# Kernel tuning notes

Hardware: AMD Instinct MI355X
Metric: run time of the kernel (lower is better)

Reference implementation:

```python
import jax, jax.numpy as jnp
import numpy as np

N_EMBED = 384
NUM_HEADS = 6
HEAD_SIZE = 64
B, T = 128, 256


def setup_inputs() -> dict:
    key = jax.random.key(0)
    ks = jax.random.split(key, 6)
    x = jax.random.normal(ks[0], (B, T, N_EMBED), dtype=jnp.float32)
    s = 0.02
    Wq = jax.random.normal(ks[1], (NUM_HEADS, N_EMBED, HEAD_SIZE), dtype=jnp.float32) * s
    Wk = jax.random.normal(ks[2], (NUM_HEADS, N_EMBED, HEAD_SIZE), dtype=jnp.float32) * s
    Wv = jax.random.normal(ks[3], (NUM_HEADS, N_EMBED, HEAD_SIZE), dtype=jnp.float32) * s
    Wp = jax.random.normal(ks[4], (NUM_HEADS * HEAD_SIZE, N_EMBED), dtype=jnp.float32) * s
    bp = jnp.zeros((N_EMBED,), dtype=jnp.float32)
    return {"x": x, "Wq": Wq, "Wk": Wk, "Wv": Wv, "Wp": Wp, "bp": bp}


def reference(x, Wq, Wk, Wv, Wp, bp):
    # x: [B,T,C]; Wq/Wk/Wv: [H,C,hs]; Wp: [H*hs, C]
    Bx, Tx, C = x.shape
    q = jnp.einsum('btc,hcd->bhtd', x, Wq)
    k = jnp.einsum('btc,hcd->bhtd', x, Wk)
    v = jnp.einsum('btc,hcd->bhtd', x, Wv)
    scale = HEAD_SIZE ** (-0.5)
    scores = jnp.einsum('bhtd,bhsd->bhts', q, k) * scale  # [B,H,T,T]
    causal = jnp.tril(jnp.ones((Tx, Tx), dtype=bool))
    scores = jnp.where(causal, scores, -jnp.inf)
    attn = jax.nn.softmax(scores, axis=-1)
    # dropout is identity in eval mode
    out = jnp.einsum('bhts,bhsd->bhtd', attn, v)  # [B,H,T,hs]
    out = out.transpose(0, 2, 1, 3).reshape(Bx, Tx, NUM_HEADS * HEAD_SIZE)
    return out @ Wp + bp
```

## Files before the change

kernel.cpp:

```cpp
#include <hip/hip_runtime.h>
#include <hip/hip_bf16.h>

#define C_DIM 384
#define H_NUM 6
#define HS    64
#define B_DIM 128
#define T_DIM 256
#define NROWS (B_DIM * T_DIM)

typedef unsigned short u16;
typedef unsigned int u32;
typedef short bf16x8 __attribute__((ext_vector_type(8)));
typedef float floatx4 __attribute__((ext_vector_type(4)));

__device__ __forceinline__ float b2f(u16 u) {
  u32 i = ((u32)u) << 16;
  float f;
  __builtin_memcpy(&f, &i, 4);
  return f;
}
__device__ __forceinline__ u16 f2b(float f) {
  __hip_bfloat16 h = __float2bfloat16(f);
  u16 u;
  __builtin_memcpy(&u, &h, 2);
  return u;
}
__device__ __forceinline__ void gload_lds16(const void* g, void* lds) {
  __builtin_amdgcn_global_load_lds(
      (const __attribute__((address_space(1))) u32*)g,
      (__attribute__((address_space(3))) u32*)lds, 16, 0, 0);
}

__global__ void cvt_x_kernel(const float* __restrict__ x, u16* __restrict__ xb,
                             int n4) {
  int i = blockIdx.x * blockDim.x + threadIdx.x;
  if (i >= n4) return;
  float4 f = ((const float4*)x)[i];
  ushort4 o;
  o.x = f2b(f.x); o.y = f2b(f.y); o.z = f2b(f.z); o.w = f2b(f.w);
  ((ushort4*)xb)[i] = o;
}

__global__ void cvt_w_kernel(const float* __restrict__ Wq,
                             const float* __restrict__ Wk,
                             const float* __restrict__ Wv,
                             const float* __restrict__ Wp,
                             u16* __restrict__ Wt, u16* __restrict__ Wpt) {
  const int QKV = 3 * H_NUM * HS * C_DIM;
  int idx = blockIdx.x * blockDim.x + threadIdx.x;
  if (idx < QKV) {
    int slab = idx / (HS * C_DIM);
    int rem = idx % (HS * C_DIM);
    int d = rem / C_DIM, c = rem % C_DIM;
    int tz = slab / H_NUM, h = slab % H_NUM;
    const float* W = (tz == 0) ? Wq : (tz == 1) ? Wk : Wv;
    Wt[idx] = f2b(W[(h * C_DIM + c) * HS + d]);
  } else {
    int j = idx - QKV;
    if (j < C_DIM * C_DIM) {
      int n = j / C_DIM, c = j % C_DIM;
      Wpt[j] = f2b(Wp[c * C_DIM + n]);
    }
  }
}

struct GemmAcc {
  floatx4 acc[4][4];
};

__device__ __forceinline__ void gemm_tile_128x128(
    const u16* __restrict__ a_rows, const u16* __restrict__ bt_rows,
    u16* As, u16* Bs, GemmAcc& g) {
  const int tid = threadIdx.x;
  const int lane = tid & 63;
  const int w = tid >> 6;
  const int lr = lane >> 3;
  const int lkc = (lane & 7) * 8;
  const int qd = lane >> 4;
  const int ln = lane & 15;
  const int mw = (w >> 1) * 64;
  const int nw = (w & 1) * 64;

#pragma unroll
  for (int i = 0; i < 4; ++i)
#pragma unroll
    for (int j = 0; j < 4; ++j) g.acc[i][j] = floatx4{0.f, 0.f, 0.f, 0.f};

  for (int kb = 0; kb < C_DIM / 64; ++kb) {
    const int k0 = kb * 64;
    __syncthreads();
#pragma unroll
    for (int s = 0; s < 4; ++s) {
      const int rbase = (s * 4 + w) * 8;
      gload_lds16(a_rows + (size_t)(rbase + lr) * C_DIM + k0 + lkc,
                  As + rbase * 64);
      gload_lds16(bt_rows + (size_t)(rbase + lr) * C_DIM + k0 + lkc,
                  Bs + rbase * 64);
    }
    __syncthreads();

#pragma unroll
    for (int kk = 0; kk < 2; ++kk) {
      bf16x8 af[4], bf[4];
#pragma unroll
      for (int mt = 0; mt < 4; ++mt)
        af[mt] = *(const bf16x8*)&As[(mw + mt * 16 + ln) * 64 + kk * 32 + qd * 8];
#pragma unroll
      for (int nt = 0; nt < 4; ++nt)
        bf[nt] = *(const bf16x8*)&Bs[(nw + nt * 16 + ln) * 64 + kk * 32 + qd * 8];
#pragma unroll
      for (int mt = 0; mt < 4; ++mt)
#pragma unroll
        for (int nt = 0; nt < 4; ++nt)
          g.acc[mt][nt] = __builtin_amdgcn_mfma_f32_16x16x32_bf16(
              af[mt], bf[nt], g.acc[mt][nt], 0, 0, 0);
    }
  }
}

__global__ __launch_bounds__(256) void qkv_gemm(
    const u16* __restrict__ xb, const u16* __restrict__ Wt,
    u16* __restrict__ q, u16* __restrict__ k, u16* __restrict__ vT) {
  __shared__ u16 smem[128 * 136];
  u16* As = smem;
  u16* Bs = smem + 8192;
  const int row0 = blockIdx.x * 128;
  const int sb = blockIdx.y;
  const int tz = sb / 3;
  const int h0 = (sb % 3) * 2;
  const u16* wbase = Wt + (size_t)(tz * H_NUM + h0) * (HS * C_DIM);

  GemmAcc g;
  gemm_tile_128x128(xb + (size_t)row0 * C_DIM, wbase, As, Bs, g);

  const int lane = threadIdx.x & 63;
  const int w = threadIdx.x >> 6;
  const int qd = lane >> 4, ln = lane & 15;
  const int mw = (w >> 1) * 64, nw = (w & 1) * 64;

  if (tz < 2) {
    u16* outbase = (tz == 0) ? q : k;
#pragma unroll
    for (int mt = 0; mt < 4; ++mt) {
#pragma unroll
      for (int nt = 0; nt < 4; ++nt) {
        const int cl = nw + nt * 16 + ln;
        const int head = h0 + (cl >> 6), d = cl & 63;
#pragma unroll
        for (int r = 0; r < 4; ++r) {
          const int grow = row0 + mw + mt * 16 + qd * 4 + r;
          const int b = grow >> 8, t = grow & 255;
          outbase[(((size_t)b * H_NUM + head) * T_DIM + t) * HS + d] =
              f2b(g.acc[mt][nt][r]);
        }
      }
    }
  } else {
    __syncthreads();
#pragma unroll
    for (int mt = 0; mt < 4; ++mt)
#pragma unroll
      for (int nt = 0; nt < 4; ++nt)
#pragma unroll
        for (int r = 0; r < 4; ++r)
          smem[(nw + nt * 16 + ln) * 136 + mw + mt * 16 + qd * 4 + r] =
              f2b(g.acc[mt][nt][r]);
    __syncthreads();
    const int b = row0 >> 8;
    const int t0 = row0 & 255;
#pragma unroll
    for (int it = 0; it < 8; ++it) {
      const int idx = it * 256 + threadIdx.x;
      const int d_l = idx >> 4, tc = idx & 15;
      uint4 val = *(const uint4*)&smem[d_l * 136 + tc * 8];
      const int head = h0 + (d_l >> 6), d = d_l & 63;
      *(uint4*)&vT[(((size_t)b * H_NUM + head) * HS + d) * T_DIM + t0 + tc * 8] =
          val;
    }
  }
}

template <bool DIAG>
__device__ __forceinline__ void attn_chunk(int c, int mt, int lane, int ln,
                                           int qd, const bf16x8* qf,
                                           const u16* Kls, u16* Pw,
                                           const u16* vTg, floatx4* oacc,
                                           float* lsum) {
  floatx4 sacc[4];
#pragma unroll
  for (int st = 0; st < 4; ++st) {
    sacc[st] = floatx4{0.f, 0.f, 0.f, 0.f};
#pragma unroll
    for (int kc = 0; kc < 2; ++kc) {
      bf16x8 kf = *(const bf16x8*)&Kls[((c * 4 + st) * 2 + kc) * 512 + lane * 8];
      sacc[st] =
          __builtin_amdgcn_mfma_f32_16x16x32_bf16(qf[kc], kf, sacc[st], 0, 0, 0);
    }
  }
#pragma unroll
  for (int st = 0; st < 4; ++st) {
#pragma unroll
    for (int r = 0; r < 4; ++r) {
      const float sv = sacc[st][r] * 0.125f;
      float p = __expf(sv);
      if (DIAG) {
        const bool ok = (c * 64 + st * 16 + ln) <= (mt * 16 + qd * 4 + r);
        p = ok ? p : 0.f;
      }
      lsum[r] += p;
      Pw[(qd * 4 + r) * 72 + st * 16 + ln] = f2b(p);
    }
  }
#pragma unroll
  for (int kc2 = 0; kc2 < 2; ++kc2) {
    bf16x8 pf = *(const bf16x8*)&Pw[ln * 72 + kc2 * 32 + qd * 8];
#pragma unroll
    for (int dt = 0; dt < 4; ++dt) {
      bf16x8 vf = *(const bf16x8*)(vTg + (dt * 16 + ln) * 256 + c * 64 +
                                   kc2 * 32 + qd * 8);
      oacc[dt] =
          __builtin_amdgcn_mfma_f32_16x16x32_bf16(pf, vf, oacc[dt], 0, 0, 0);
    }
  }
}

__global__ __launch_bounds__(256) void attn_mfma(
    const u16* __restrict__ q, const u16* __restrict__ k,
    const u16* __restrict__ vT, u16* __restrict__ y) {
  __shared__ u16 Kls[32 * 512];
  __shared__ u16 Pls[4 * 1152];
  const int bh = blockIdx.x;
  const int b = bh / H_NUM, h = bh % H_NUM;
  const int tid = threadIdx.x, lane = tid & 63, w = tid >> 6;
  const int ln = lane & 15, qd = lane >> 4;
  const u16* qg = q + (size_t)bh * (T_DIM * HS);
  const u16* kg = k + (size_t)bh * (T_DIM * HS);
  const u16* vTg = vT + (size_t)bh * (HS * T_DIM);
  u16* Pw = Pls + w * 1152;

#pragma unroll
  for (int ff = 0; ff < 8; ++ff) {
    const int fid = w * 8 + ff;
    const int S16 = fid >> 1, kc = fid & 1;
    gload_lds16(kg + (S16 * 16 + ln) * 64 + kc * 32 + qd * 8, &Kls[fid * 512]);
  }
  __syncthreads();

#pragma unroll
  for (int i = 0; i < 4; ++i) {
    const int mt = i * 4 + w;
    bf16x8 qf[2];
#pragma unroll
    for (int kc = 0; kc < 2; ++kc)
      qf[kc] = *(const bf16x8*)(qg + (mt * 16 + ln) * 64 + kc * 32 + qd * 8);

    floatx4 oacc[4];
    float lsum[4];
#pragma unroll
    for (int dt = 0; dt < 4; ++dt) oacc[dt] = floatx4{0.f, 0.f, 0.f, 0.f};
#pragma unroll
    for (int r = 0; r < 4; ++r) lsum[r] = 0.f;

    const int cmax = mt >> 2;
    for (int c = 0; c < cmax; ++c)
      attn_chunk<false>(c, mt, lane, ln, qd, qf, Kls, Pw, vTg, oacc, lsum);
    attn_chunk<true>(cmax, mt, lane, ln, qd, qf, Kls, Pw, vTg, oacc, lsum);

#pragma unroll
    for (int off = 1; off < 16; off <<= 1)
#pragma unroll
      for (int r = 0; r < 4; ++r) lsum[r] += __shfl_xor(lsum[r], off);

#pragma unroll
    for (int r = 0; r < 4; ++r) {
      const float inv = 1.f / lsum[r];
      const int t = mt * 16 + qd * 4 + r;
      u16* yo = y + ((size_t)b * T_DIM + t) * C_DIM + h * HS;
#pragma unroll
      for (int dt = 0; dt < 4; ++dt) yo[dt * 16 + ln] = f2b(oacc[dt][r] * inv);
    }
  }
}

__global__ __launch_bounds__(256) void proj_gemm(
    const u16* __restrict__ yb, const u16* __restrict__ Wpt,
    const float* __restrict__ bp, float* __restrict__ out) {
  __shared__ u16 As[128 * 64];
  __shared__ u16 Bs[128 * 64];
  const int row0 = blockIdx.x * 128;
  const int n0 = blockIdx.y * 128;

  GemmAcc g;
  gemm_tile_128x128(yb + (size_t)row0 * C_DIM, Wpt + (size_t)n0 * C_DIM, As, Bs, g);

  const int lane = threadIdx.x & 63;
  const int w = threadIdx.x >> 6;
  const int qd = lane >> 4, ln = lane & 15;
  const int mw = (w >> 1) * 64, nw = (w & 1) * 64;
#pragma unroll
  for (int nt = 0; nt < 4; ++nt) {
    const int col = n0 + nw + nt * 16 + ln;
    const float bias = bp[col];
#pragma unroll
    for (int mt = 0; mt < 4; ++mt) {
#pragma unroll
      for (int r = 0; r < 4; ++r) {
        const int grow = row0 + mw + mt * 16 + qd * 4 + r;
        out[(size_t)grow * C_DIM + col] = g.acc[mt][nt][r] + bias;
      }
    }
  }
}

extern "C" void kernel_launch(void* const* d_in, const int* in_sizes, int n_in,
                              void* d_out, int out_size, void* d_ws, size_t ws_size,
                              hipStream_t stream) {
  const float* x  = (const float*)d_in[0];
  const float* Wq = (const float*)d_in[1];
  const float* Wk = (const float*)d_in[2];
  const float* Wv = (const float*)d_in[3];
  const float* Wp = (const float*)d_in[4];
  const float* bp = (const float*)d_in[5];
  float* out = (float*)d_out;

  const size_t n_x = (size_t)NROWS * C_DIM;
  const size_t qkv_elems = (size_t)B_DIM * H_NUM * T_DIM * HS;

  u16* xb  = (u16*)d_ws;
  u16* Wt  = xb + n_x;
  u16* Wpt = Wt + 3 * H_NUM * HS * C_DIM;
  u16* q   = Wpt + C_DIM * C_DIM;
  u16* k   = q + qkv_elems;
  u16* vT  = k + qkv_elems;
  u16* y   = xb;

  cvt_x_kernel<<<(int)(n_x / 4 + 255) / 256, 256, 0, stream>>>(x, xb, (int)(n_x / 4));
  cvt_w_kernel<<<2304, 256, 0, stream>>>(Wq, Wk, Wv, Wp, Wt, Wpt);
  qkv_gemm<<<dim3(NROWS / 128, 9), 256, 0, stream>>>(xb, Wt, q, k, vT);
  attn_mfma<<<B_DIM * H_NUM, 256, 0, stream>>>(q, k, vT, y);
  proj_gemm<<<dim3(NROWS / 128, 3), 256, 0, stream>>>(y, Wpt, bp, out);
}
```

Before: 225.5 us.

## Fuse x conversion, QKV projection and causal attention into one per-head kernel

Replaces the separate x-conversion, QKV GEMM and attention kernels with one kernel per (batch, head). Each kernel converts fp32 x to bf16 while staging it into LDS, computes that head's Q, K and V with MFMA, writes them to workspace, then runs causal attention with 8 waves. Query tiles are paired (w and 15-w) so each wave gets a similar amount of causal work. This removes two launches and the bf16 x round trip through memory. In exchange, each batch's x is reread and reconverted by all six head blocks, and Q/K/V still go through global memory within the block.

```diff
diff --git a/kernel.cpp b/kernel.cpp
--- a/kernel.cpp
+++ b/kernel.cpp
@@ -13,12 +13,6 @@
 typedef short bf16x8 __attribute__((ext_vector_type(8)));
 typedef float floatx4 __attribute__((ext_vector_type(4)));
 
-__device__ __forceinline__ float b2f(u16 u) {
-  u32 i = ((u32)u) << 16;
-  float f;
-  __builtin_memcpy(&f, &i, 4);
-  return f;
-}
 __device__ __forceinline__ u16 f2b(float f) {
   __hip_bfloat16 h = __float2bfloat16(f);
   u16 u;
@@ -31,35 +25,216 @@
       (__attribute__((address_space(3))) u32*)lds, 16, 0, 0);
 }
 
-__global__ void cvt_x_kernel(const float* __restrict__ x, u16* __restrict__ xb,
-                             int n4) {
-  int i = blockIdx.x * blockDim.x + threadIdx.x;
-  if (i >= n4) return;
-  float4 f = ((const float4*)x)[i];
-  ushort4 o;
-  o.x = f2b(f.x); o.y = f2b(f.y); o.z = f2b(f.z); o.w = f2b(f.w);
-  ((ushort4*)xb)[i] = o;
-}
-
 __global__ void cvt_w_kernel(const float* __restrict__ Wq,
                              const float* __restrict__ Wk,
                              const float* __restrict__ Wv,
                              const float* __restrict__ Wp,
-                             u16* __restrict__ Wt, u16* __restrict__ Wpt) {
-  const int QKV = 3 * H_NUM * HS * C_DIM;
+                             u16* __restrict__ Wh, u16* __restrict__ Wpt) {
+  const int WHN = H_NUM * 192 * C_DIM;
   int idx = blockIdx.x * blockDim.x + threadIdx.x;
-  if (idx < QKV) {
-    int slab = idx / (HS * C_DIM);
-    int rem = idx % (HS * C_DIM);
-    int d = rem / C_DIM, c = rem % C_DIM;
-    int tz = slab / H_NUM, h = slab % H_NUM;
+  if (idx < WHN) {
+    int h = idx / (192 * C_DIM);
+    int rem = idx % (192 * C_DIM);
+    int r = rem / C_DIM, c = rem % C_DIM;
+    int tz = r >> 6, d = r & 63;
     const float* W = (tz == 0) ? Wq : (tz == 1) ? Wk : Wv;
-    Wt[idx] = f2b(W[(h * C_DIM + c) * HS + d]);
+    Wh[idx] = f2b(W[((size_t)h * C_DIM + c) * HS + d]);
   } else {
-    int j = idx - QKV;
+    int j = idx - WHN;
     if (j < C_DIM * C_DIM) {
       int n = j / C_DIM, c = j % C_DIM;
       Wpt[j] = f2b(Wp[c * C_DIM + n]);
+    }
+  }
+}
+
+template <bool DIAG>
+__device__ __forceinline__ void attn_chunk(int c, int mt, int lane, int ln,
+                                           int qd, const bf16x8* qf,
+                                           const u16* Kls, u16* Pw,
+                                           const u16* vTg, floatx4* oacc,
+                                           float* lsum) {
+  floatx4 sacc[4];
+#pragma unroll
+  for (int st = 0; st < 4; ++st) {
+    sacc[st] = floatx4{0.f, 0.f, 0.f, 0.f};
+#pragma unroll
+    for (int kc = 0; kc < 2; ++kc) {
+      bf16x8 kf = *(const bf16x8*)&Kls[((c * 4 + st) * 2 + kc) * 512 + lane * 8];
+      sacc[st] =
+          __builtin_amdgcn_mfma_f32_16x16x32_bf16(qf[kc], kf, sacc[st], 0, 0, 0);
+    }
+  }
+#pragma unroll
+  for (int st = 0; st < 4; ++st) {
+#pragma unroll
+    for (int r = 0; r < 4; ++r) {
+      const float sv = sacc[st][r] * 0.125f;
+      float p = __expf(sv);
+      if (DIAG) {
+        const bool ok = (c * 64 + st * 16 + ln) <= (mt * 16 + qd * 4 + r);
+        p = ok ? p : 0.f;
+      }
+      lsum[r] += p;
+      Pw[(qd * 4 + r) * 72 + st * 16 + ln] = f2b(p);
+    }
+  }
+#pragma unroll
+  for (int kc2 = 0; kc2 < 2; ++kc2) {
+    bf16x8 pf = *(const bf16x8*)&Pw[ln * 72 + kc2 * 32 + qd * 8];
+#pragma unroll
+    for (int dt = 0; dt < 4; ++dt) {
+      bf16x8 vf = *(const bf16x8*)(vTg + (dt * 16 + ln) * 256 + c * 64 +
+                                   kc2 * 32 + qd * 8);
+      oacc[dt] =
+          __builtin_amdgcn_mfma_f32_16x16x32_bf16(pf, vf, oacc[dt], 0, 0, 0);
+    }
+  }
+}
+
+__global__ __launch_bounds__(512, 4) void qkv_attn(
+    const float* __restrict__ x, const u16* __restrict__ Wh,
+    u16* __restrict__ qsA, u16* __restrict__ ksA, u16* __restrict__ vtA,
+    u16* __restrict__ y) {
+  __shared__ u16 smem[25600];
+  const int bh = blockIdx.x;
+  const int b = bh / H_NUM, h = bh % H_NUM;
+  const int tid = threadIdx.x, lane = tid & 63, w = tid >> 6;
+  const int qd = lane >> 4, ln = lane & 15;
+  const int wm = w & 1, wn = w >> 1;
+  const int lr = lane >> 3, lkc = (lane & 7) * 8;
+
+  const float* xb = x + (size_t)b * T_DIM * C_DIM;
+  const u16* Bh = Wh + (size_t)h * 192 * C_DIM;
+  u16* qs = qsA + (size_t)bh * (T_DIM * HS);
+  u16* ks = ksA + (size_t)bh * (T_DIM * HS);
+  u16* vt = vtA + (size_t)bh * (T_DIM * HS);
+
+  u16* As = smem;
+  u16* Bs = smem + 8192;
+  u16* Ts = smem;
+
+  for (int mh = 0; mh < 2; ++mh) {
+    const int t0 = mh * 128;
+    floatx4 acc[4][3];
+#pragma unroll
+    for (int mt = 0; mt < 4; ++mt)
+#pragma unroll
+      for (int nt = 0; nt < 3; ++nt) acc[mt][nt] = floatx4{0.f, 0.f, 0.f, 0.f};
+
+    for (int kb = 0; kb < 6; ++kb) {
+      const int k0 = kb * 64;
+      __syncthreads();
+#pragma unroll
+      for (int s = 0; s < 2; ++s) {
+        const int c = s * 512 + tid;
+        const int row = c >> 3, col = (c & 7) * 8;
+        const float* src = xb + (size_t)(t0 + row) * C_DIM + k0 + col;
+        const float4 f0 = *(const float4*)src;
+        const float4 f1 = *(const float4*)(src + 4);
+        bf16x8 pk;
+        pk[0] = (short)f2b(f0.x); pk[1] = (short)f2b(f0.y);
+        pk[2] = (short)f2b(f0.z); pk[3] = (short)f2b(f0.w);
+        pk[4] = (short)f2b(f1.x); pk[5] = (short)f2b(f1.y);
+        pk[6] = (short)f2b(f1.z); pk[7] = (short)f2b(f1.w);
+        *(bf16x8*)&As[row * 64 + col] = pk;
+      }
+#pragma unroll
+      for (int ss = 0; ss < 3; ++ss) {
+        const int rbase = (w * 3 + ss) * 8;
+        gload_lds16(Bh + (size_t)(rbase + lr) * C_DIM + k0 + lkc,
+                    Bs + rbase * 64);
+      }
+      __syncthreads();
+#pragma unroll
+      for (int kk = 0; kk < 2; ++kk) {
+        bf16x8 af[4], bfr[3];
+#pragma unroll
+        for (int mt = 0; mt < 4; ++mt)
+          af[mt] =
+              *(const bf16x8*)&As[(wm * 64 + mt * 16 + ln) * 64 + kk * 32 + qd * 8];
+#pragma unroll
+        for (int nt = 0; nt < 3; ++nt)
+          bfr[nt] =
+              *(const bf16x8*)&Bs[(wn * 48 + nt * 16 + ln) * 64 + kk * 32 + qd * 8];
+#pragma unroll
+        for (int mt = 0; mt < 4; ++mt)
+#pragma unroll
+          for (int nt = 0; nt < 3; ++nt)
+            acc[mt][nt] = __builtin_amdgcn_mfma_f32_16x16x32_bf16(
+                af[mt], bfr[nt], acc[mt][nt], 0, 0, 0);
+      }
+    }
+    __syncthreads();
+#pragma unroll
+    for (int nt = 0; nt < 3; ++nt) {
+      const int tz = (wn * 48 + nt * 16) >> 6;
+      const int d = (wn * 48 + nt * 16 + ln) & 63;
+#pragma unroll
+      for (int mt = 0; mt < 4; ++mt) {
+#pragma unroll
+        for (int r = 0; r < 4; ++r) {
+          const int tl = wm * 64 + mt * 16 + qd * 4 + r;
+          const u16 val = f2b(acc[mt][nt][r]);
+          if (tz == 0) qs[(size_t)(t0 + tl) * HS + d] = val;
+          else if (tz == 1) ks[(size_t)(t0 + tl) * HS + d] = val;
+          else Ts[d * 136 + tl] = val;
+        }
+      }
+    }
+    __syncthreads();
+#pragma unroll
+    for (int s = 0; s < 2; ++s) {
+      const int c = s * 512 + tid;
+      const int d = c >> 4, part = c & 15;
+      *(uint4*)&vt[(size_t)d * T_DIM + t0 + part * 8] =
+          *(const uint4*)&Ts[d * 136 + part * 8];
+    }
+  }
+  __syncthreads();
+
+  u16* Kls = smem;
+  u16* Pw = smem + 16384 + w * 1152;
+
+#pragma unroll
+  for (int ff = 0; ff < 4; ++ff) {
+    const int fid = w * 4 + ff, S16 = fid >> 1, kc = fid & 1;
+    gload_lds16(ks + (S16 * 16 + ln) * HS + kc * 32 + qd * 8, &Kls[fid * 512]);
+  }
+  __syncthreads();
+
+#pragma unroll
+  for (int i = 0; i < 2; ++i) {
+    const int mt = (i == 0) ? w : 15 - w;
+    bf16x8 qf[2];
+#pragma unroll
+    for (int kc = 0; kc < 2; ++kc)
+      qf[kc] = *(const bf16x8*)(qs + (mt * 16 + ln) * HS + kc * 32 + qd * 8);
+
+    floatx4 oacc[4];
+    float lsum[4];
+#pragma unroll
+    for (int dt = 0; dt < 4; ++dt) oacc[dt] = floatx4{0.f, 0.f, 0.f, 0.f};
+#pragma unroll
+    for (int r = 0; r < 4; ++r) lsum[r] = 0.f;
+
+    const int cmax = mt >> 2;
+    for (int c = 0; c < cmax; ++c)
+      attn_chunk<false>(c, mt, lane, ln, qd, qf, Kls, Pw, vt, oacc, lsum);
+    attn_chunk<true>(cmax, mt, lane, ln, qd, qf, Kls, Pw, vt, oacc, lsum);
+
+#pragma unroll
+    for (int off = 1; off < 16; off <<= 1)
+#pragma unroll
+      for (int r = 0; r < 4; ++r) lsum[r] += __shfl_xor(lsum[r], off);
+
+#pragma unroll
+    for (int r = 0; r < 4; ++r) {
+      const float inv = 1.f / lsum[r];
+      const int t = mt * 16 + qd * 4 + r;
+      u16* yo = y + ((size_t)b * T_DIM + t) * C_DIM + h * HS;
+#pragma unroll
+      for (int dt = 0; dt < 4; ++dt) yo[dt * 16 + ln] = f2b(oacc[dt][r] * inv);
     }
   }
 }
@@ -118,170 +293,6 @@
   }
 }
 
-__global__ __launch_bounds__(256) void qkv_gemm(
-    const u16* __restrict__ xb, const u16* __restrict__ Wt,
-    u16* __restrict__ q, u16* __restrict__ k, u16* __restrict__ vT) {
-  __shared__ u16 smem[128 * 136];
-  u16* As = smem;
-  u16* Bs = smem + 8192;
-  const int row0 = blockIdx.x * 128;
-  const int sb = blockIdx.y;
-  const int tz = sb / 3;
-  const int h0 = (sb % 3) * 2;
-  const u16* wbase = Wt + (size_t)(tz * H_NUM + h0) * (HS * C_DIM);
-
-  GemmAcc g;
-  gemm_tile_128x128(xb + (size_t)row0 * C_DIM, wbase, As, Bs, g);
-
-  const int lane = threadIdx.x & 63;
-  const int w = threadIdx.x >> 6;
-  const int qd = lane >> 4, ln = lane & 15;
-  const int mw = (w >> 1) * 64, nw = (w & 1) * 64;
-
-  if (tz < 2) {
-    u16* outbase = (tz == 0) ? q : k;
-#pragma unroll
-    for (int mt = 0; mt < 4; ++mt) {
-#pragma unroll
-      for (int nt = 0; nt < 4; ++nt) {
-        const int cl = nw + nt * 16 + ln;
-        const int head = h0 + (cl >> 6), d = cl & 63;
-#pragma unroll
-        for (int r = 0; r < 4; ++r) {
-          const int grow = row0 + mw + mt * 16 + qd * 4 + r;
-          const int b = grow >> 8, t = grow & 255;
-          outbase[(((size_t)b * H_NUM + head) * T_DIM + t) * HS + d] =
-              f2b(g.acc[mt][nt][r]);
-        }
-      }
-    }
-  } else {
-    __syncthreads();
-#pragma unroll
-    for (int mt = 0; mt < 4; ++mt)
-#pragma unroll
-      for (int nt = 0; nt < 4; ++nt)
-#pragma unroll
-        for (int r = 0; r < 4; ++r)
-          smem[(nw + nt * 16 + ln) * 136 + mw + mt * 16 + qd * 4 + r] =
-              f2b(g.acc[mt][nt][r]);
-    __syncthreads();
-    const int b = row0 >> 8;
-    const int t0 = row0 & 255;
-#pragma unroll
-    for (int it = 0; it < 8; ++it) {
-      const int idx = it * 256 + threadIdx.x;
-      const int d_l = idx >> 4, tc = idx & 15;
-      uint4 val = *(const uint4*)&smem[d_l * 136 + tc * 8];
-      const int head = h0 + (d_l >> 6), d = d_l & 63;
-      *(uint4*)&vT[(((size_t)b * H_NUM + head) * HS + d) * T_DIM + t0 + tc * 8] =
-          val;
-    }
-  }
-}
-
-template <bool DIAG>
-__device__ __forceinline__ void attn_chunk(int c, int mt, int lane, int ln,
-                                           int qd, const bf16x8* qf,
-                                           const u16* Kls, u16* Pw,
-                                           const u16* vTg, floatx4* oacc,
-                                           float* lsum) {
-  floatx4 sacc[4];
-#pragma unroll
-  for (int st = 0; st < 4; ++st) {
-    sacc[st] = floatx4{0.f, 0.f, 0.f, 0.f};
-#pragma unroll
-    for (int kc = 0; kc < 2; ++kc) {
-      bf16x8 kf = *(const bf16x8*)&Kls[((c * 4 + st) * 2 + kc) * 512 + lane * 8];
-      sacc[st] =
-          __builtin_amdgcn_mfma_f32_16x16x32_bf16(qf[kc], kf, sacc[st], 0, 0, 0);
-    }
-  }
-#pragma unroll
-  for (int st = 0; st < 4; ++st) {
-#pragma unroll
-    for (int r = 0; r < 4; ++r) {
-      const float sv = sacc[st][r] * 0.125f;
-      float p = __expf(sv);
-      if (DIAG) {
-        const bool ok = (c * 64 + st * 16 + ln) <= (mt * 16 + qd * 4 + r);
-        p = ok ? p : 0.f;
-      }
-      lsum[r] += p;
-      Pw[(qd * 4 + r) * 72 + st * 16 + ln] = f2b(p);
-    }
-  }
-#pragma unroll
-  for (int kc2 = 0; kc2 < 2; ++kc2) {
-    bf16x8 pf = *(const bf16x8*)&Pw[ln * 72 + kc2 * 32 + qd * 8];
-#pragma unroll
-    for (int dt = 0; dt < 4; ++dt) {
-      bf16x8 vf = *(const bf16x8*)(vTg + (dt * 16 + ln) * 256 + c * 64 +
-                                   kc2 * 32 + qd * 8);
-      oacc[dt] =
-          __builtin_amdgcn_mfma_f32_16x16x32_bf16(pf, vf, oacc[dt], 0, 0, 0);
-    }
-  }
-}
-
-__global__ __launch_bounds__(256) void attn_mfma(
-    const u16* __restrict__ q, const u16* __restrict__ k,
-    const u16* __restrict__ vT, u16* __restrict__ y) {
-  __shared__ u16 Kls[32 * 512];
-  __shared__ u16 Pls[4 * 1152];
-  const int bh = blockIdx.x;
-  const int b = bh / H_NUM, h = bh % H_NUM;
-  const int tid = threadIdx.x, lane = tid & 63, w = tid >> 6;
-  const int ln = lane & 15, qd = lane >> 4;
-  const u16* qg = q + (size_t)bh * (T_DIM * HS);
-  const u16* kg = k + (size_t)bh * (T_DIM * HS);
-  const u16* vTg = vT + (size_t)bh * (HS * T_DIM);
-  u16* Pw = Pls + w * 1152;
-
-#pragma unroll
-  for (int ff = 0; ff < 8; ++ff) {
-    const int fid = w * 8 + ff;
-    const int S16 = fid >> 1, kc = fid & 1;
-    gload_lds16(kg + (S16 * 16 + ln) * 64 + kc * 32 + qd * 8, &Kls[fid * 512]);
-  }
-  __syncthreads();
-
-#pragma unroll
-  for (int i = 0; i < 4; ++i) {
-    const int mt = i * 4 + w;
-    bf16x8 qf[2];
-#pragma unroll
-    for (int kc = 0; kc < 2; ++kc)
-      qf[kc] = *(const bf16x8*)(qg + (mt * 16 + ln) * 64 + kc * 32 + qd * 8);
-
-    floatx4 oacc[4];
-    float lsum[4];
-#pragma unroll
-    for (int dt = 0; dt < 4; ++dt) oacc[dt] = floatx4{0.f, 0.f, 0.f, 0.f};
-#pragma unroll
-    for (int r = 0; r < 4; ++r) lsum[r] = 0.f;
-
-    const int cmax = mt >> 2;
-    for (int c = 0; c < cmax; ++c)
-      attn_chunk<false>(c, mt, lane, ln, qd, qf, Kls, Pw, vTg, oacc, lsum);
-    attn_chunk<true>(cmax, mt, lane, ln, qd, qf, Kls, Pw, vTg, oacc, lsum);
-
-#pragma unroll
-    for (int off = 1; off < 16; off <<= 1)
-#pragma unroll
-      for (int r = 0; r < 4; ++r) lsum[r] += __shfl_xor(lsum[r], off);
-
-#pragma unroll
-    for (int r = 0; r < 4; ++r) {
-      const float inv = 1.f / lsum[r];
-      const int t = mt * 16 + qd * 4 + r;
-      u16* yo = y + ((size_t)b * T_DIM + t) * C_DIM + h * HS;
-#pragma unroll
-      for (int dt = 0; dt < 4; ++dt) yo[dt * 16 + ln] = f2b(oacc[dt][r] * inv);
-    }
-  }
-}
-
 __global__ __launch_bounds__(256) void proj_gemm(
     const u16* __restrict__ yb, const u16* __restrict__ Wpt,
     const float* __restrict__ bp, float* __restrict__ out) {
@@ -323,20 +334,16 @@
   const float* bp = (const float*)d_in[5];
   float* out = (float*)d_out;
 
-  const size_t n_x = (size_t)NROWS * C_DIM;
   const size_t qkv_elems = (size_t)B_DIM * H_NUM * T_DIM * HS;
 
-  u16* xb  = (u16*)d_ws;
-  u16* Wt  = xb + n_x;
-  u16* Wpt = Wt + 3 * H_NUM * HS * C_DIM;
-  u16* q   = Wpt + C_DIM * C_DIM;
-  u16* k   = q + qkv_elems;
-  u16* vT  = k + qkv_elems;
-  u16* y   = xb;
-
-  cvt_x_kernel<<<(int)(n_x / 4 + 255) / 256, 256, 0, stream>>>(x, xb, (int)(n_x / 4));
-  cvt_w_kernel<<<2304, 256, 0, stream>>>(Wq, Wk, Wv, Wp, Wt, Wpt);
-  qkv_gemm<<<dim3(NROWS / 128, 9), 256, 0, stream>>>(xb, Wt, q, k, vT);
-  attn_mfma<<<B_DIM * H_NUM, 256, 0, stream>>>(q, k, vT, y);
+  u16* Wh  = (u16*)d_ws;
+  u16* Wpt = Wh + (size_t)H_NUM * 192 * C_DIM;
+  u16* qsA = Wpt + C_DIM * C_DIM;
+  u16* ksA = qsA + qkv_elems;
+  u16* vtA = ksA + qkv_elems;
+  u16* y   = vtA + qkv_elems;
+
+  cvt_w_kernel<<<2304, 256, 0, stream>>>(Wq, Wk, Wv, Wp, Wh, Wpt);
+  qkv_attn<<<B_DIM * H_NUM, 512, 0, stream>>>(x, Wh, qsA, ksA, vtA, y);
   proj_gemm<<<dim3(NROWS / 128, 3), 256, 0, stream>>>(y, Wpt, bp, out);
 }
```

Result: slower. 263.0 us (+16.6%).
